# Performance work log

Hardware: AMD Instinct MI355X
Metric: run time of the kernel (lower is better)

The kernel has to match this reference:

```python
import jax, jax.numpy as jnp
import numpy as np


def setup_inputs() -> dict:
    key = jax.random.key(0)
    k1, k2, k3 = jax.random.split(key, 3)
    n_tokens, model_dim, num_experts, top_k = 32768, 2048, 256, 8
    return {
        "hidden_states": jax.random.normal(k1, (n_tokens, model_dim), dtype=jnp.float16),
        "router_logits": jax.random.normal(k2, (n_tokens, num_experts), dtype=jnp.float32),
        "e_score_correction_bias": jax.random.normal(k3, (num_experts,), dtype=jnp.float32),
        "top_k": top_k,
    }


def reference(hidden_states, router_logits, e_score_correction_bias, top_k):
    # DeepSeek-V3-style biased top-k gating (fused kernel semantics):
    #  - sigmoid scoring of router logits
    #  - expert selection on score + correction bias (bias affects selection only)
    #  - routing weights are the ORIGINAL sigmoid scores, renormalized over top_k
    #  - expert_counts histogram and per-token offsets (rank among tokens routed
    #    to the same expert, in flattened row-major order)
    num_experts = router_logits.shape[1]
    s = jax.nn.sigmoid(router_logits)                      # [T, E] fp32
    sel = s + e_score_correction_bias[None, :]             # selection scores
    _, idx = jax.lax.top_k(sel, top_k)                     # [T, K] int32
    scores = jnp.take_along_axis(s, idx, axis=1)           # [T, K]
    scores = scores / jnp.sum(scores, axis=1, keepdims=True)
    # histogram + exclusive per-expert running count -> offsets
    flat = idx.reshape(-1)                                 # [T*K]
    onehot = (flat[:, None] == jnp.arange(num_experts, dtype=idx.dtype)[None, :]).astype(jnp.int32)
    csum = jnp.cumsum(onehot, axis=0)                      # inclusive counts [T*K, E]
    expert_counts = csum[-1]                               # [E]
    excl = csum - onehot                                   # exclusive counts
    offsets = jnp.take_along_axis(excl, flat[:, None], axis=1)[:, 0].reshape(idx.shape)
    return scores, idx.astype(jnp.int32), expert_counts, offsets.astype(jnp.int32)
```

## Files before the change

### kernel.cpp

```cpp
#include <hip/hip_runtime.h>
#include <hip/hip_bf16.h>
#include <math.h>


constexpr int E = 256;
constexpr int K = 8;
constexpr int TOK_PER_CHUNK = 128;
constexpr int CHUNK_ELEMS = TOK_PER_CHUNK * K;

__global__ __launch_bounds__(256) void topk_kernel(
    const float* __restrict__ logits,
    const float* __restrict__ bias,
    float* __restrict__ out_scores,
    float* __restrict__ out_idx,
    int*   __restrict__ ws_idx,
    int T)
{
    const int wave = (blockIdx.x * blockDim.x + threadIdx.x) >> 6;
    const int lane = threadIdx.x & 63;
    if (wave >= T) return;

    const float4 x = reinterpret_cast<const float4*>(logits + (size_t)wave * E)[lane];
    const float4 b = reinterpret_cast<const float4*>(bias)[lane];

    float s0 = 1.f / (1.f + expf(-x.x));
    float s1 = 1.f / (1.f + expf(-x.y));
    float s2 = 1.f / (1.f + expf(-x.z));
    float s3 = 1.f / (1.f + expf(-x.w));
    float sel0 = s0 + b.x;
    float sel1 = s1 + b.y;
    float sel2 = s2 + b.z;
    float sel3 = s3 + b.w;

    float sc[K];
    int   id[K];
    float sum = 0.f;

    #pragma unroll
    for (int r = 0; r < K; ++r) {
        float bv = sel0; int bi = lane * 4;
        if (sel1 > bv) { bv = sel1; bi = lane * 4 + 1; }
        if (sel2 > bv) { bv = sel2; bi = lane * 4 + 2; }
        if (sel3 > bv) { bv = sel3; bi = lane * 4 + 3; }
        #pragma unroll
        for (int off = 32; off; off >>= 1) {
            float ov = __shfl_xor(bv, off, 64);
            int   oi = __shfl_xor(bi, off, 64);
            if (ov > bv || (ov == bv && oi < bi)) { bv = ov; bi = oi; }
        }
        const int j = bi & 3, src = bi >> 2;
        float cand = (j == 0) ? s0 : (j == 1) ? s1 : (j == 2) ? s2 : s3;
        float sv = __shfl(cand, src, 64);
        sc[r] = sv; id[r] = bi; sum += sv;
        if (lane == src) {
            if      (j == 0) sel0 = -INFINITY;
            else if (j == 1) sel1 = -INFINITY;
            else if (j == 2) sel2 = -INFINITY;
            else             sel3 = -INFINITY;
        }
    }

    if (lane == 0) {
        const size_t o = (size_t)wave * K;
        float4 a = make_float4(sc[0] / sum, sc[1] / sum, sc[2] / sum, sc[3] / sum);
        float4 c = make_float4(sc[4] / sum, sc[5] / sum, sc[6] / sum, sc[7] / sum);
        *reinterpret_cast<float4*>(out_scores + o)     = a;
        *reinterpret_cast<float4*>(out_scores + o + 4) = c;
        float4 fi0 = make_float4((float)id[0], (float)id[1], (float)id[2], (float)id[3]);
        float4 fi1 = make_float4((float)id[4], (float)id[5], (float)id[6], (float)id[7]);
        *reinterpret_cast<float4*>(out_idx + o)     = fi0;
        *reinterpret_cast<float4*>(out_idx + o + 4) = fi1;
        int4 w0 = make_int4(id[0], id[1], id[2], id[3]);
        int4 w1 = make_int4(id[4], id[5], id[6], id[7]);
        *reinterpret_cast<int4*>(ws_idx + o)     = w0;
        *reinterpret_cast<int4*>(ws_idx + o + 4) = w1;
    }
}

__global__ __launch_bounds__(256) void hist_kernel(
    const int* __restrict__ ws_idx,
    int* __restrict__ cnt,
    int total)
{
    __shared__ int h[E];
    h[threadIdx.x] = 0;
    __syncthreads();
    const int base = blockIdx.x * CHUNK_ELEMS;
    const int n = min(CHUNK_ELEMS, total - base);
    for (int p = threadIdx.x; p < n; p += 256)
        atomicAdd(&h[ws_idx[base + p]], 1);
    __syncthreads();
    cnt[blockIdx.x * E + threadIdx.x] = h[threadIdx.x];
}

__global__ __launch_bounds__(256) void scan_kernel(
    const int* __restrict__ cnt,
    int* __restrict__ baseoff,
    float* __restrict__ out_counts,
    int nchunk)
{
    const int e = blockIdx.x;
    const int b = threadIdx.x;
    __shared__ int v[256];
    const int c = (b < nchunk) ? cnt[b * E + e] : 0;
    v[b] = c;
    __syncthreads();
    #pragma unroll
    for (int off = 1; off < 256; off <<= 1) {
        int t = (b >= off) ? v[b - off] : 0;
        __syncthreads();
        v[b] += t;
        __syncthreads();
    }
    const int incl = v[b];
    if (b < nchunk) baseoff[b * E + e] = incl - c;
    if (b == 255) out_counts[e] = (float)incl;
}

__global__ __launch_bounds__(256) void offs_kernel(
    const int* __restrict__ ws_idx,
    const int* __restrict__ baseoff,
    float* __restrict__ out_off,
    int total)
{
    __shared__ int sidx[CHUNK_ELEMS];
    const int base = blockIdx.x * CHUNK_ELEMS;
    const int n = min(CHUNK_ELEMS, total - base);
    for (int p = threadIdx.x; p < n; p += 256)
        sidx[p] = ws_idx[base + p];
    const int e = threadIdx.x;
    int c = baseoff[blockIdx.x * E + e];
    __syncthreads();
    for (int p = 0; p < n; ++p) {
        int v = sidx[p];
        if (v == e) { out_off[base + p] = (float)c; ++c; }
    }
}

extern "C" void kernel_launch(void* const* d_in, const int* in_sizes, int n_in,
                              void* d_out, int out_size, void* d_ws, size_t ws_size,
                              hipStream_t stream) {
    const float* logits = (const float*)d_in[1];
    const float* bias   = (const float*)d_in[2];
    const int T = in_sizes[1] / E;
    const int total = T * K;
    const int nchunk = (T + TOK_PER_CHUNK - 1) / TOK_PER_CHUNK;

    float* out        = (float*)d_out;
    float* out_scores = out;
    float* out_idx    = out + (size_t)total;
    float* out_counts = out + 2 * (size_t)total;
    float* out_off    = out_counts + E;

    int* ws_idx  = (int*)d_ws;
    int* cnt     = ws_idx + total;
    int* baseoff = cnt + nchunk * E;

    topk_kernel<<<(T + 3) / 4, 256, 0, stream>>>(logits, bias, out_scores, out_idx, ws_idx, T);
    hist_kernel<<<nchunk, 256, 0, stream>>>(ws_idx, cnt, total);
    scan_kernel<<<E, 256, 0, stream>>>(cnt, baseoff, out_counts, nchunk);
    offs_kernel<<<nchunk, 256, 0, stream>>>(ws_idx, baseoff, out_off, total);
}
```

Before: 407.6 us.

## Fuse histogram into top-k kernel and shrink chunks for parallel offset pass

Computes per-chunk expert histograms inside the top-k kernel using shared-memory atomics, removing the separate histogram pass and its reread of indices. Chunks shrink to 16 tokens so the serial per-expert offset loop is much shorter and has many more blocks. The scan kernel now handles up to 2048 chunks by having each thread do 8 chunks serially before the block scan. The trade-off is a larger count/base-offset workspace and more scan traffic.

```diff
diff --git a/kernel.cpp b/kernel.cpp
--- a/kernel.cpp
+++ b/kernel.cpp
@@ -5,92 +5,98 @@
 
 constexpr int E = 256;
 constexpr int K = 8;
-constexpr int TOK_PER_CHUNK = 128;
-constexpr int CHUNK_ELEMS = TOK_PER_CHUNK * K;
+constexpr int TOK_PER_BLK = 16;
+constexpr int CHUNK_ELEMS = TOK_PER_BLK * K;
+constexpr int MAX_CHUNKS = 2048;
 
-__global__ __launch_bounds__(256) void topk_kernel(
+__global__ __launch_bounds__(1024) void topk_hist_kernel(
     const float* __restrict__ logits,
     const float* __restrict__ bias,
     float* __restrict__ out_scores,
     float* __restrict__ out_idx,
     int*   __restrict__ ws_idx,
+    int*   __restrict__ cnt,
     int T)
 {
-    const int wave = (blockIdx.x * blockDim.x + threadIdx.x) >> 6;
-    const int lane = threadIdx.x & 63;
-    if (wave >= T) return;
+    __shared__ int h[E];
+    const int tid = threadIdx.x;
+    if (tid < E) h[tid] = 0;
+    __syncthreads();
 
-    const float4 x = reinterpret_cast<const float4*>(logits + (size_t)wave * E)[lane];
-    const float4 b = reinterpret_cast<const float4*>(bias)[lane];
-
-    float s0 = 1.f / (1.f + expf(-x.x));
-    float s1 = 1.f / (1.f + expf(-x.y));
-    float s2 = 1.f / (1.f + expf(-x.z));
-    float s3 = 1.f / (1.f + expf(-x.w));
-    float sel0 = s0 + b.x;
-    float sel1 = s1 + b.y;
-    float sel2 = s2 + b.z;
-    float sel3 = s3 + b.w;
+    const int wid  = tid >> 6;
+    const int lane = tid & 63;
+    const int token = blockIdx.x * TOK_PER_BLK + wid;
+    const bool active = token < T;
 
     float sc[K];
     int   id[K];
     float sum = 0.f;
 
-    #pragma unroll
-    for (int r = 0; r < K; ++r) {
-        float bv = sel0; int bi = lane * 4;
-        if (sel1 > bv) { bv = sel1; bi = lane * 4 + 1; }
-        if (sel2 > bv) { bv = sel2; bi = lane * 4 + 2; }
-        if (sel3 > bv) { bv = sel3; bi = lane * 4 + 3; }
+    if (active) {
+        const float4 x = reinterpret_cast<const float4*>(logits + (size_t)token * E)[lane];
+        const float4 b = reinterpret_cast<const float4*>(bias)[lane];
+        float s0 = 1.f / (1.f + __expf(-x.x));
+        float s1 = 1.f / (1.f + __expf(-x.y));
+        float s2 = 1.f / (1.f + __expf(-x.z));
+        float s3 = 1.f / (1.f + __expf(-x.w));
+        float sel0 = s0 + b.x, sel1 = s1 + b.y, sel2 = s2 + b.z, sel3 = s3 + b.w;
+
         #pragma unroll
-        for (int off = 32; off; off >>= 1) {
-            float ov = __shfl_xor(bv, off, 64);
-            int   oi = __shfl_xor(bi, off, 64);
-            if (ov > bv || (ov == bv && oi < bi)) { bv = ov; bi = oi; }
+        for (int r = 0; r < K; ++r) {
+            float bv = sel0; int bi = lane * 4;
+            if (sel1 > bv) { bv = sel1; bi = lane * 4 + 1; }
+            if (sel2 > bv) { bv = sel2; bi = lane * 4 + 2; }
+            if (sel3 > bv) { bv = sel3; bi = lane * 4 + 3; }
+            #pragma unroll
+            for (int off = 32; off; off >>= 1) {
+                float ov = __shfl_xor(bv, off, 64);
+                int   oi = __shfl_xor(bi, off, 64);
+                if (ov > bv || (ov == bv && oi < bi)) { bv = ov; bi = oi; }
+            }
+            const int j = bi & 3, src = bi >> 2;
+            float cand = (j == 0) ? s0 : (j == 1) ? s1 : (j == 2) ? s2 : s3;
+            float sv = __shfl(cand, src, 64);
+            sc[r] = sv; id[r] = bi; sum += sv;
+            if (lane == src) {
+                if      (j == 0) sel0 = -INFINITY;
+                else if (j == 1) sel1 = -INFINITY;
+                else if (j == 2) sel2 = -INFINITY;
+                else             sel3 = -INFINITY;
+            }
         }
-        const int j = bi & 3, src = bi >> 2;
-        float cand = (j == 0) ? s0 : (j == 1) ? s1 : (j == 2) ? s2 : s3;
-        float sv = __shfl(cand, src, 64);
-        sc[r] = sv; id[r] = bi; sum += sv;
-        if (lane == src) {
-            if      (j == 0) sel0 = -INFINITY;
-            else if (j == 1) sel1 = -INFINITY;
-            else if (j == 2) sel2 = -INFINITY;
-            else             sel3 = -INFINITY;
+
+        if (lane < 8) {
+            int v = id[0];
+            if (lane == 1) v = id[1];
+            if (lane == 2) v = id[2];
+            if (lane == 3) v = id[3];
+            if (lane == 4) v = id[4];
+            if (lane == 5) v = id[5];
+            if (lane == 6) v = id[6];
+            if (lane == 7) v = id[7];
+            atomicAdd(&h[v], 1);
+        }
+
+        if (lane == 0) {
+            const size_t o = (size_t)token * K;
+            float inv = 1.f / sum;
+            float4 a = make_float4(sc[0] * inv, sc[1] * inv, sc[2] * inv, sc[3] * inv);
+            float4 c = make_float4(sc[4] * inv, sc[5] * inv, sc[6] * inv, sc[7] * inv);
+            *reinterpret_cast<float4*>(out_scores + o)     = a;
+            *reinterpret_cast<float4*>(out_scores + o + 4) = c;
+            float4 f0 = make_float4((float)id[0], (float)id[1], (float)id[2], (float)id[3]);
+            float4 f1 = make_float4((float)id[4], (float)id[5], (float)id[6], (float)id[7]);
+            *reinterpret_cast<float4*>(out_idx + o)     = f0;
+            *reinterpret_cast<float4*>(out_idx + o + 4) = f1;
+            int4 w0 = make_int4(id[0], id[1], id[2], id[3]);
+            int4 w1 = make_int4(id[4], id[5], id[6], id[7]);
+            *reinterpret_cast<int4*>(ws_idx + o)     = w0;
+            *reinterpret_cast<int4*>(ws_idx + o + 4) = w1;
         }
     }
 
-    if (lane == 0) {
-        const size_t o = (size_t)wave * K;
-        float4 a = make_float4(sc[0] / sum, sc[1] / sum, sc[2] / sum, sc[3] / sum);
-        float4 c = make_float4(sc[4] / sum, sc[5] / sum, sc[6] / sum, sc[7] / sum);
-        *reinterpret_cast<float4*>(out_scores + o)     = a;
-        *reinterpret_cast<float4*>(out_scores + o + 4) = c;
-        float4 fi0 = make_float4((float)id[0], (float)id[1], (float)id[2], (float)id[3]);
-        float4 fi1 = make_float4((float)id[4], (float)id[5], (float)id[6], (float)id[7]);
-        *reinterpret_cast<float4*>(out_idx + o)     = fi0;
-        *reinterpret_cast<float4*>(out_idx + o + 4) = fi1;
-        int4 w0 = make_int4(id[0], id[1], id[2], id[3]);
-        int4 w1 = make_int4(id[4], id[5], id[6], id[7]);
-        *reinterpret_cast<int4*>(ws_idx + o)     = w0;
-        *reinterpret_cast<int4*>(ws_idx + o + 4) = w1;
-    }
-}
-
-__global__ __launch_bounds__(256) void hist_kernel(
-    const int* __restrict__ ws_idx,
-    int* __restrict__ cnt,
-    int total)
-{
-    __shared__ int h[E];
-    h[threadIdx.x] = 0;
     __syncthreads();
-    const int base = blockIdx.x * CHUNK_ELEMS;
-    const int n = min(CHUNK_ELEMS, total - base);
-    for (int p = threadIdx.x; p < n; p += 256)
-        atomicAdd(&h[ws_idx[base + p]], 1);
-    __syncthreads();
-    cnt[blockIdx.x * E + threadIdx.x] = h[threadIdx.x];
+    if (tid < E) cnt[(size_t)blockIdx.x * E + tid] = h[tid];
 }
 
 __global__ __launch_bounds__(256) void scan_kernel(
@@ -101,20 +107,34 @@
 {
     const int e = blockIdx.x;
     const int b = threadIdx.x;
-    __shared__ int v[256];
-    const int c = (b < nchunk) ? cnt[b * E + e] : 0;
-    v[b] = c;
+
+    int lps[8];
+    int lp = 0;
+    #pragma unroll
+    for (int j = 0; j < 8; ++j) {
+        const int c = 8 * b + j;
+        int v = (c < nchunk) ? cnt[(size_t)c * E + e] : 0;
+        lps[j] = lp;
+        lp += v;
+    }
+
+    __shared__ int s[256];
+    s[b] = lp;
     __syncthreads();
     #pragma unroll
     for (int off = 1; off < 256; off <<= 1) {
-        int t = (b >= off) ? v[b - off] : 0;
+        int t = (b >= off) ? s[b - off] : 0;
         __syncthreads();
-        v[b] += t;
+        s[b] += t;
         __syncthreads();
     }
-    const int incl = v[b];
-    if (b < nchunk) baseoff[b * E + e] = incl - c;
-    if (b == 255) out_counts[e] = (float)incl;
+    const int excl = s[b] - lp;
+    #pragma unroll
+    for (int j = 0; j < 8; ++j) {
+        const int c = 8 * b + j;
+        if (c < nchunk) baseoff[(size_t)c * E + e] = excl + lps[j];
+    }
+    if (b == 255) out_counts[e] = (float)s[255];
 }
 
 __global__ __launch_bounds__(256) void offs_kernel(
@@ -126,14 +146,12 @@
     __shared__ int sidx[CHUNK_ELEMS];
     const int base = blockIdx.x * CHUNK_ELEMS;
     const int n = min(CHUNK_ELEMS, total - base);
-    for (int p = threadIdx.x; p < n; p += 256)
-        sidx[p] = ws_idx[base + p];
+    if ((int)threadIdx.x < n) sidx[threadIdx.x] = ws_idx[base + threadIdx.x];
     const int e = threadIdx.x;
-    int c = baseoff[blockIdx.x * E + e];
+    int c = baseoff[(size_t)blockIdx.x * E + e];
     __syncthreads();
     for (int p = 0; p < n; ++p) {
-        int v = sidx[p];
-        if (v == e) { out_off[base + p] = (float)c; ++c; }
+        if (sidx[p] == e) { out_off[base + p] = (float)c; ++c; }
     }
 }
 
@@ -144,7 +162,8 @@
     const float* bias   = (const float*)d_in[2];
     const int T = in_sizes[1] / E;
     const int total = T * K;
-    const int nchunk = (T + TOK_PER_CHUNK - 1) / TOK_PER_CHUNK;
+    const int nchunk = (T + TOK_PER_BLK - 1) / TOK_PER_BLK;
+    (void)MAX_CHUNKS;
 
     float* out        = (float*)d_out;
     float* out_scores = out;
@@ -154,10 +173,10 @@
 
     int* ws_idx  = (int*)d_ws;
     int* cnt     = ws_idx + total;
-    int* baseoff = cnt + nchunk * E;
+    int* baseoff = cnt + (size_t)nchunk * E;
 
-    topk_kernel<<<(T + 3) / 4, 256, 0, stream>>>(logits, bias, out_scores, out_idx, ws_idx, T);
-    hist_kernel<<<nchunk, 256, 0, stream>>>(ws_idx, cnt, total);
+    topk_hist_kernel<<<nchunk, 1024, 0, stream>>>(logits, bias, out_scores, out_idx,
+                                                  ws_idx, cnt, T);
     scan_kernel<<<E, 256, 0, stream>>>(cnt, baseoff, out_counts, nchunk);
     offs_kernel<<<nchunk, 256, 0, stream>>>(ws_idx, baseoff, out_off, total);
 }
```

Result: faster. 385.6 us (-5.4%).
